# Kernel tuning notes

Measured on AMD Instinct MI355X. Metric: run time of the kernel, lower is better.

The kernel has to match this reference:

```python
import jax, jax.numpy as jnp
import numpy as np


def setup_inputs() -> dict:
    key = jax.random.key(0)
    k1, k2, k3 = jax.random.split(key, 3)
    B, H, N, D = 4, 16, 4096, 128
    return {
        "q": jax.random.normal(k1, (B, H, N, D), dtype=jnp.float32),
        "k": jax.random.normal(k2, (B, H, N, D), dtype=jnp.float32),
        "v": jax.random.normal(k3, (B, H, N, D), dtype=jnp.float32),
    }


def reference(q, k, v):
    # Aaren-style numerically stable online-softmax linear-attention scan.
    # q, k, v: [B, H, N, D]
    scale = 1.0
    B, H, N, D = q.shape
    qs = jnp.moveaxis(q * scale, 2, 0)  # [N, B, H, D] time-major
    ks = jnp.moveaxis(k, 2, 0)
    vs = jnp.moveaxis(v, 2, 0)

    n0 = jnp.zeros((B, H, D), dtype=q.dtype)
    d0 = jnp.zeros((B, H, 1), dtype=q.dtype)
    m0 = jnp.full((B, H, 1), -jnp.inf, dtype=q.dtype)

    def step(carry, inp):
        n_p, d_p, m_p = carry
        q_t, k_t, v_t = inp
        alpha = jnp.sum(q_t * k_t, axis=-1, keepdims=True)  # [B, H, 1]
        m_t = jnp.maximum(m_p, alpha)
        exp_mdiff = jnp.exp(m_p - m_t)
        exp_adiff = jnp.exp(alpha - m_t)
        d_t = exp_mdiff * d_p + exp_adiff
        n_t = exp_mdiff * n_p + exp_adiff * v_t
        y_t = n_t / d_t
        return (n_t, d_t, m_t), y_t

    _, y = jax.lax.scan(step, (n0, d0, m0), (qs, ks, vs))  # y: [N, B, H, D]
    return jnp.moveaxis(y, 0, 2)  # [B, H, N, D]
```

## Files before the change

### kernel.cpp

```cpp
#include <hip/hip_runtime.h>
#include <math.h>

static constexpr int ROWS = 64;
static constexpr int NSEQ = 4096;
static constexpr int DIM  = 128;
static constexpr int SC   = 32;
static constexpr int SPR  = NSEQ / SC;
static constexpr int NSC  = ROWS * SPR;
static constexpr int VC   = 64;
static constexpr int VPR  = NSEQ / VC;
static constexpr int NVC  = ROWS * VPR;

__global__ __launch_bounds__(256) void k_alpha(
    const float* __restrict__ q, const float* __restrict__ k,
    float* __restrict__ alpha, float* __restrict__ cM, float* __restrict__ cD)
{
    const int lane = threadIdx.x & 63;
    const int tile = blockIdx.x * 4 + (threadIdx.x >> 6);
    const float4* qrow = (const float4*)(q + (size_t)tile * (64 * DIM) + lane * DIM);
    const float4* krow = (const float4*)(k + (size_t)tile * (64 * DIM) + lane * DIM);

    float ax = 0.f, ay = 0.f, az = 0.f, aw = 0.f;
    for (int u0 = 0; u0 < DIM / 4; u0 += 8) {
        float4 qa[8], ka[8];
        #pragma unroll
        for (int u = 0; u < 8; ++u) qa[u] = qrow[u0 + u];
        #pragma unroll
        for (int u = 0; u < 8; ++u) ka[u] = krow[u0 + u];
        #pragma unroll
        for (int u = 0; u < 8; ++u) {
            ax += qa[u].x * ka[u].x;  ay += qa[u].y * ka[u].y;
            az += qa[u].z * ka[u].z;  aw += qa[u].w * ka[u].w;
        }
    }
    const float a = (ax + ay) + (az + aw);

    float mRun = a;
    #pragma unroll
    for (int m = 16; m >= 1; m >>= 1) mRun = fmaxf(mRun, __shfl_xor(mRun, m));
    float e = __expf(a - mRun);
    #pragma unroll
    for (int m = 16; m >= 1; m >>= 1) e += __shfl_xor(e, m);

    alpha[tile * 64 + lane] = a;
    if ((lane & 31) == 0) {
        const int s = tile * 2 + (lane >> 5);
        cM[s] = mRun; cD[s] = e;
    }
}

__global__ __launch_bounds__(256) void k_scan(
    const float* __restrict__ alpha, const float* __restrict__ cM,
    const float* __restrict__ cD,
    float* __restrict__ pM, float* __restrict__ pD, float2* __restrict__ coefCW)
{
    __shared__ float lM[SPR], lD[SPR], lpM[SPR], lpD[SPR];
    const int row  = blockIdx.x;
    const int lane = threadIdx.x & 31;
    const int g    = threadIdx.x >> 5;

    if (threadIdx.x < SPR) {
        lM[threadIdx.x] = cM[row * SPR + threadIdx.x];
        lD[threadIdx.x] = cD[row * SPR + threadIdx.x];
    }
    __syncthreads();

    if (threadIdx.x == 0) {
        float m = -INFINITY, d = 0.f;
        for (int sl = 0; sl < SPR; ++sl) {
            lpM[sl] = m; lpD[sl] = d;
            pM[row * SPR + sl] = m; pD[row * SPR + sl] = d;
            const float M = lM[sl], D = lD[sl];
            const float mn = fmaxf(m, M);
            d = d * __expf(m - mn) + D * __expf(M - mn);
            m = mn;
        }
    }
    __syncthreads();

    for (int sl = g; sl < SPR; sl += 8) {
        const int s = row * SPR + sl;
        const float a = alpha[s * SC + lane];
        float m = lpM[sl];
        float cK = 0.f, wK = 0.f;
        for (int t = 0; t < SC; ++t) {
            const float at = __shfl(a, t, 32);
            const float mn = fmaxf(m, at);
            const float c  = __expf(m - mn);
            const float w  = __expf(at - mn);
            cK = (t == lane) ? c : cK;
            wK = (t == lane) ? w : wK;
            m = mn;
        }
        coefCW[s * SC + lane] = make_float2(cK, wK);
    }
}

__global__ __launch_bounds__(256) void k_agg(
    const float* __restrict__ v, const float2* __restrict__ coefCW,
    float2* __restrict__ aggN)
{
    const int lane  = threadIdx.x & 63;
    const int C     = blockIdx.x * 4 + (threadIdx.x >> 6);
    const int vbase = C * (VC * DIM);
    const int cbase = __builtin_amdgcn_readfirstlane(C * VC);

    float nx = 0.f, ny = 0.f;
    for (int t0 = 0; t0 < VC; t0 += 8) {
        float2 cw[8], vv[8];
        #pragma unroll
        for (int u = 0; u < 8; ++u) cw[u] = coefCW[cbase + t0 + u];
        #pragma unroll
        for (int u = 0; u < 8; ++u)
            vv[u] = *((const float2*)(v + vbase + (t0 + u) * DIM) + lane);
        #pragma unroll
        for (int u = 0; u < 8; ++u) {
            nx = cw[u].x * nx + cw[u].y * vv[u].x;
            ny = cw[u].x * ny + cw[u].y * vv[u].y;
        }
    }
    aggN[C * (DIM / 2) + lane] = make_float2(nx, ny);
}

__global__ __launch_bounds__(128) void k_pref(
    float* __restrict__ aggN, const float* __restrict__ pM)
{
    const int row = blockIdx.x;
    const int d   = threadIdx.x;
    float state = 0.f;
    for (int C0 = 0; C0 < VPR; C0 += 8) {
        float nb[8], f1[8];
        #pragma unroll
        for (int u = 0; u < 8; ++u) {
            const int C = C0 + u;
            nb[u] = aggN[(row * VPR + C) * DIM + d];
            const int Cg = row * VPR + C;
            const float mp  = pM[2 * Cg];
            const bool last = (C == VPR - 1);
            const float mp2 = last ? 0.f : pM[2 * Cg + 2];
            f1[u] = last ? 0.f : __expf(mp - mp2);
        }
        #pragma unroll
        for (int u = 0; u < 8; ++u) {
            const float nc = nb[u];
            aggN[(row * VPR + C0 + u) * DIM + d] = state;
            state = state * f1[u] + nc;
        }
    }
}

__global__ __launch_bounds__(256) void k_out(
    const float* __restrict__ v, const float2* __restrict__ coefCW,
    const float2* __restrict__ preN, const float* __restrict__ pD,
    float* __restrict__ y)
{
    const int lane  = threadIdx.x & 63;
    const int C     = blockIdx.x * 4 + (threadIdx.x >> 6);
    const int vbase = C * (VC * DIM);
    const int cbase = __builtin_amdgcn_readfirstlane(C * VC);

    float2 n  = preN[C * (DIM / 2) + lane];
    float dch = pD[2 * C];

    for (int t0 = 0; t0 < VC; t0 += 8) {
        float2 cw[8], vv[8];
        #pragma unroll
        for (int u = 0; u < 8; ++u) cw[u] = coefCW[cbase + t0 + u];
        #pragma unroll
        for (int u = 0; u < 8; ++u)
            vv[u] = *((const float2*)(v + vbase + (t0 + u) * DIM) + lane);
        #pragma unroll
        for (int u = 0; u < 8; ++u) {
            n.x = cw[u].x * n.x + cw[u].y * vv[u].x;
            n.y = cw[u].x * n.y + cw[u].y * vv[u].y;
            dch = cw[u].x * dch + cw[u].y;
            const float rd = __builtin_amdgcn_rcpf(dch);
            *((float2*)(y + vbase + (t0 + u) * DIM) + lane) =
                make_float2(n.x * rd, n.y * rd);
        }
    }
}

extern "C" void kernel_launch(void* const* d_in, const int* in_sizes, int n_in,
                              void* d_out, int out_size, void* d_ws, size_t ws_size,
                              hipStream_t stream) {
    const float* q = (const float*)d_in[0];
    const float* k = (const float*)d_in[1];
    const float* v = (const float*)d_in[2];
    float* y  = (float*)d_out;
    float* ws = (float*)d_ws;

    float*  coefCWf = ws;
    float*  pM      = coefCWf + 2 * ROWS * NSEQ;
    float*  pD      = pM + NSC;
    float*  cM      = pD + NSC;
    float*  cD      = cM + NSC;
    float*  U       = cD + NSC;
    float*  alphaA  = U;
    float*  aggNf   = U;
    float2* coefCW  = (float2*)coefCWf;
    float2* aggN2   = (float2*)aggNf;

    k_alpha<<<(ROWS * NSEQ / 64) / 4, 256, 0, stream>>>(q, k, alphaA, cM, cD);
    k_scan<<<ROWS, 256, 0, stream>>>(alphaA, cM, cD, pM, pD, coefCW);
    k_agg<<<NVC / 4, 256, 0, stream>>>(v, coefCW, aggN2);
    k_pref<<<ROWS, DIM, 0, stream>>>(aggNf, pM);
    k_out<<<NVC / 4, 256, 0, stream>>>(v, coefCW, aggN2, pD, y);
}
```

Baseline: 191.3 us.

## Stage q/k tiles via global_load_lds with swizzle and parallelize chunk max scan

k_alpha now copies 32-row q and k tiles straight into LDS with direct global-to-LDS loads, using an XOR swizzle. Four lanes then work on each dot product from LDS, replacing the old pattern where each thread read a strided 512-byte row and got poorly coalesced accesses. The scan chunk size drops from 32 to 16. The serial per-lane max/exp loop in k_scan becomes a log-step shuffle prefix max, and the chunk indexing in k_pref and k_out changes to match. The costs are more serial-scan chunks per row for thread 0 and extra LDS traffic.

```diff
diff --git a/kernel.cpp b/kernel.cpp
--- a/kernel.cpp
+++ b/kernel.cpp
@@ -1,52 +1,73 @@
 #include <hip/hip_runtime.h>
 #include <math.h>
+#include <stdint.h>
 
 static constexpr int ROWS = 64;
 static constexpr int NSEQ = 4096;
 static constexpr int DIM  = 128;
-static constexpr int SC   = 32;
+static constexpr int SC   = 16;
 static constexpr int SPR  = NSEQ / SC;
 static constexpr int NSC  = ROWS * SPR;
 static constexpr int VC   = 64;
 static constexpr int VPR  = NSEQ / VC;
 static constexpr int NVC  = ROWS * VPR;
-
-__global__ __launch_bounds__(256) void k_alpha(
+static constexpr int SPC  = VC / SC;
+
+typedef __attribute__((address_space(3))) uint32_t  lds_u32;
+typedef const __attribute__((address_space(1))) uint32_t g_u32;
+
+__global__ __launch_bounds__(128) void k_alpha(
     const float* __restrict__ q, const float* __restrict__ k,
     float* __restrict__ alpha, float* __restrict__ cM, float* __restrict__ cD)
 {
-    const int lane = threadIdx.x & 63;
-    const int tile = blockIdx.x * 4 + (threadIdx.x >> 6);
-    const float4* qrow = (const float4*)(q + (size_t)tile * (64 * DIM) + lane * DIM);
-    const float4* krow = (const float4*)(k + (size_t)tile * (64 * DIM) + lane * DIM);
-
-    float ax = 0.f, ay = 0.f, az = 0.f, aw = 0.f;
-    for (int u0 = 0; u0 < DIM / 4; u0 += 8) {
-        float4 qa[8], ka[8];
-        #pragma unroll
-        for (int u = 0; u < 8; ++u) qa[u] = qrow[u0 + u];
-        #pragma unroll
-        for (int u = 0; u < 8; ++u) ka[u] = krow[u0 + u];
-        #pragma unroll
-        for (int u = 0; u < 8; ++u) {
-            ax += qa[u].x * ka[u].x;  ay += qa[u].y * ka[u].y;
-            az += qa[u].z * ka[u].z;  aw += qa[u].w * ka[u].w;
-        }
-    }
-    const float a = (ax + ay) + (az + aw);
-
-    float mRun = a;
-    #pragma unroll
-    for (int m = 16; m >= 1; m >>= 1) mRun = fmaxf(mRun, __shfl_xor(mRun, m));
-    float e = __expf(a - mRun);
-    #pragma unroll
-    for (int m = 16; m >= 1; m >>= 1) e += __shfl_xor(e, m);
-
-    alpha[tile * 64 + lane] = a;
-    if ((lane & 31) == 0) {
-        const int s = tile * 2 + (lane >> 5);
-        cM[s] = mRun; cD[s] = e;
-    }
+    __shared__ float lds[8192];
+    const int l    = threadIdx.x & 63;
+    const int w    = threadIdx.x >> 6;
+    const int tile = blockIdx.x;
+    const int b4   = tile * (32 * DIM);
+
+    #pragma unroll
+    for (int i = 0; i < 8; ++i) {
+        const int p  = w * 8192 + i * 1024 + l * 16;
+        const int ps = p ^ (((p >> 9) & 7) << 4);
+        __builtin_amdgcn_global_load_lds((g_u32*)(q + b4 + (ps >> 2)),
+                                         (lds_u32*)&lds[(w * 8192 + i * 1024) >> 2],
+                                         16, 0, 0);
+    }
+    #pragma unroll
+    for (int i = 0; i < 8; ++i) {
+        const int p  = w * 8192 + i * 1024 + l * 16;
+        const int ps = p ^ (((p >> 9) & 7) << 4);
+        __builtin_amdgcn_global_load_lds((g_u32*)(k + b4 + (ps >> 2)),
+                                         (lds_u32*)&lds[4096 + ((w * 8192 + i * 1024) >> 2)],
+                                         16, 0, 0);
+    }
+    asm volatile("s_waitcnt vmcnt(0)" ::: "memory");
+    __syncthreads();
+
+    const int tl = w * 16 + (l >> 2);
+    const int c  = l & 3;
+    const int sw = (tl & 7) << 4;
+    float acc = 0.f;
+    #pragma unroll
+    for (int j = 0; j < 8; ++j) {
+        const int off = tl * 512 + ((c * 128 + j * 16) ^ sw);
+        const float4 qv = *(const float4*)((const char*)lds + off);
+        const float4 kv = *(const float4*)((const char*)lds + 16384 + off);
+        acc += qv.x * kv.x + qv.y * kv.y + qv.z * kv.z + qv.w * kv.w;
+    }
+    acc += __shfl_xor(acc, 1);
+    acc += __shfl_xor(acc, 2);
+
+    float M = acc;
+    #pragma unroll
+    for (int m = 4; m <= 32; m <<= 1) M = fmaxf(M, __shfl_xor(M, m));
+    float e = (c == 0) ? __expf(acc - M) : 0.f;
+    #pragma unroll
+    for (int m = 4; m <= 32; m <<= 1) e += __shfl_xor(e, m);
+
+    if (c == 0) alpha[tile * 32 + tl] = acc;
+    if (l == 0) { cM[tile * 2 + w] = M; cD[tile * 2 + w] = e; }
 }
 
 __global__ __launch_bounds__(256) void k_scan(
@@ -54,21 +75,18 @@
     const float* __restrict__ cD,
     float* __restrict__ pM, float* __restrict__ pD, float2* __restrict__ coefCW)
 {
-    __shared__ float lM[SPR], lD[SPR], lpM[SPR], lpD[SPR];
-    const int row  = blockIdx.x;
-    const int lane = threadIdx.x & 31;
-    const int g    = threadIdx.x >> 5;
-
-    if (threadIdx.x < SPR) {
-        lM[threadIdx.x] = cM[row * SPR + threadIdx.x];
-        lD[threadIdx.x] = cD[row * SPR + threadIdx.x];
-    }
+    __shared__ float lM[SPR], lD[SPR], lpM[SPR];
+    const int row = blockIdx.x;
+    const int tid = threadIdx.x;
+
+    lM[tid] = cM[row * SPR + tid];
+    lD[tid] = cD[row * SPR + tid];
     __syncthreads();
 
-    if (threadIdx.x == 0) {
+    if (tid == 0) {
         float m = -INFINITY, d = 0.f;
         for (int sl = 0; sl < SPR; ++sl) {
-            lpM[sl] = m; lpD[sl] = d;
+            lpM[sl] = m;
             pM[row * SPR + sl] = m; pD[row * SPR + sl] = d;
             const float M = lM[sl], D = lD[sl];
             const float mn = fmaxf(m, M);
@@ -78,21 +96,23 @@
     }
     __syncthreads();
 
-    for (int sl = g; sl < SPR; sl += 8) {
+    const int li = tid & 15, grp = tid >> 4;
+    for (int sl = grp; sl < SPR; sl += 16) {
         const int s = row * SPR + sl;
-        const float a = alpha[s * SC + lane];
-        float m = lpM[sl];
-        float cK = 0.f, wK = 0.f;
-        for (int t = 0; t < SC; ++t) {
-            const float at = __shfl(a, t, 32);
-            const float mn = fmaxf(m, at);
-            const float c  = __expf(m - mn);
-            const float w  = __expf(at - mn);
-            cK = (t == lane) ? c : cK;
-            wK = (t == lane) ? w : wK;
-            m = mn;
-        }
-        coefCW[s * SC + lane] = make_float2(cK, wK);
+        const float a = alpha[s * SC + li];
+        float m = a;
+        #pragma unroll
+        for (int d = 1; d < 16; d <<= 1) {
+            const float o = __shfl_up(m, d, 16);
+            if (li >= d) m = fmaxf(m, o);
+        }
+        const float carry = lpM[sl];
+        const float mf = fmaxf(m, carry);
+        float mp = __shfl_up(mf, 1, 16);
+        if (li == 0) mp = carry;
+        const float cc = __expf(mp - mf);
+        const float wt = __expf(a - mf);
+        coefCW[s * SC + li] = make_float2(cc, wt);
     }
 }
 
@@ -132,12 +152,12 @@
         float nb[8], f1[8];
         #pragma unroll
         for (int u = 0; u < 8; ++u) {
-            const int C = C0 + u;
-            nb[u] = aggN[(row * VPR + C) * DIM + d];
+            const int C  = C0 + u;
             const int Cg = row * VPR + C;
-            const float mp  = pM[2 * Cg];
+            nb[u] = aggN[Cg * DIM + d];
             const bool last = (C == VPR - 1);
-            const float mp2 = last ? 0.f : pM[2 * Cg + 2];
+            const float mp  = pM[SPC * Cg];
+            const float mp2 = last ? 0.f : pM[SPC * Cg + SPC];
             f1[u] = last ? 0.f : __expf(mp - mp2);
         }
         #pragma unroll
@@ -160,7 +180,7 @@
     const int cbase = __builtin_amdgcn_readfirstlane(C * VC);
 
     float2 n  = preN[C * (DIM / 2) + lane];
-    float dch = pD[2 * C];
+    float dch = pD[SPC * C];
 
     for (int t0 = 0; t0 < VC; t0 += 8) {
         float2 cw[8], vv[8];
@@ -201,7 +221,7 @@
     float2* coefCW  = (float2*)coefCWf;
     float2* aggN2   = (float2*)aggNf;
 
-    k_alpha<<<(ROWS * NSEQ / 64) / 4, 256, 0, stream>>>(q, k, alphaA, cM, cD);
+    k_alpha<<<ROWS * NSEQ / 32, 128, 0, stream>>>(q, k, alphaA, cM, cD);
     k_scan<<<ROWS, 256, 0, stream>>>(alphaA, cM, cD, pM, pD, coefCW);
     k_agg<<<NVC / 4, 256, 0, stream>>>(v, coefCW, aggN2);
     k_pref<<<ROWS, DIM, 0, stream>>>(aggNf, pM);
```

Result: faster. 159.6 us (-16.6%).
